# Performance work log

Measured on AMD Instinct MI355X. Metric: run time of the kernel, lower is better.

Reference implementation:

```python
import jax, jax.numpy as jnp
import numpy as np

N_NODES = 100000


def gcn_conv(x, W, b, src, tgt, n_nodes):
    """PyG GCNConv: add self-loops, symmetric deg^-1/2 normalization, then aggregate."""
    xw = x @ W  # [N, out]
    # degree including self-loop (edge weights are all 1)
    deg = jnp.zeros((n_nodes,), dtype=x.dtype).at[tgt].add(1.0) + 1.0
    dinv = deg ** -0.5
    norm = dinv[src] * dinv[tgt]  # [E]
    agg = jax.ops.segment_sum(xw[src] * norm[:, None], tgt, num_segments=n_nodes)
    # self-loop contribution: norm_ii = dinv_i^2
    return agg + xw * (dinv ** 2)[:, None] + b


def setup_inputs() -> dict:
    key = jax.random.key(0)
    ks = jax.random.split(key, 9)
    d_in, d_hid, d_out = 128, 128, 64
    x = jax.random.normal(ks[0], (N_NODES, d_in), dtype=jnp.float32)
    edge_index = jax.random.randint(ks[1], (2, 200000), 0, N_NODES)
    pos_edge_index = jax.random.randint(ks[2], (2, 500000), 0, N_NODES)
    s = lambda k, shape, fan: jax.random.normal(k, shape, dtype=jnp.float32) / np.sqrt(fan)
    return {
        "x": x,
        "edge_index": edge_index,
        "pos_edge_index": pos_edge_index,
        "W_init": s(ks[3], (d_in, d_in), d_in),
        "b_init": jnp.zeros((d_in,), dtype=jnp.float32),
        "W1": s(ks[4], (d_in, d_hid), d_in),
        "b1": jnp.zeros((d_hid,), dtype=jnp.float32),
        "W2": s(ks[5], (d_hid, d_out), d_hid),
        "b2": jnp.zeros((d_out,), dtype=jnp.float32),
    }


def reference(x, edge_index, pos_edge_index, W_init, b_init, W1, b1, W2, b2):
    n = x.shape[0]
    src, tgt = pos_edge_index[0], pos_edge_index[1]
    h = x @ W_init + b_init                      # init_linear
    h = gcn_conv(h, W1, b1, src, tgt, n)         # conv1
    h = jax.nn.relu(h)
    h = gcn_conv(h, W2, b2, src, tgt, n)         # conv2
    # edge dot-product scoring (use_bilinear=False)
    logits = jnp.sum(h[edge_index[0]] * h[edge_index[1]], axis=-1)  # [E_pred]
    return logits
```

## Files before the change

### kernel.cpp

```cpp
#include <hip/hip_runtime.h>


typedef __attribute__((ext_vector_type(8))) short short8;
typedef __attribute__((ext_vector_type(4))) float f32x4;

__device__ __forceinline__ ushort f2bf(float v) {
    unsigned u = __float_as_uint(v);
    return (ushort)((u + 0x7FFFu + ((u >> 16) & 1u)) >> 16);
}
__device__ __forceinline__ float bf2f(ushort b) {
    return __uint_as_float(((unsigned)b) << 16);
}
__device__ __forceinline__ float bflo(unsigned u) { return __uint_as_float(u << 16); }
__device__ __forceinline__ float bfhi(unsigned u) { return __uint_as_float(u & 0xFFFF0000u); }
__device__ __forceinline__ unsigned packbf(float x, float y) {
    return (unsigned)f2bf(x) | ((unsigned)f2bf(y) << 16);
}
__device__ __forceinline__ void split2(float v, ushort& h, ushort& l) {
    unsigned u = __float_as_uint(v);
    unsigned hb = (u + 0x7FFFu + ((u >> 16) & 1u)) & 0xFFFF0000u;
    h = (ushort)(hb >> 16);
    l = f2bf(v - __uint_as_float(hb));
}

__global__ void prep_kernel(const float* __restrict__ Wi, const float* __restrict__ W1,
                            const float* __restrict__ W2,
                            ushort* __restrict__ Ti, ushort* __restrict__ T1,
                            ushort* __restrict__ T2, int* __restrict__ zp, int ztot)
{
    int o = blockIdx.x * blockDim.x + threadIdx.x;
    if (o < ztot) zp[o] = 0;
    if (o < 16384) {
        int c = o >> 7, k = o & 127;
        Ti[o] = f2bf(Wi[(size_t)k * 128 + c]);
    } else if (o < 32768) {
        int p = o - 16384;
        int c = p >> 7, k = p & 127;
        T1[p] = f2bf(W1[(size_t)k * 128 + c]);
    } else if (o < 40960) {
        int p = o - 32768;
        int c = p >> 7, k = p & 127;
        T2[p] = f2bf(W2[(size_t)k * 64 + c]);
    }
}

__global__ void hist_kernel(const int* __restrict__ tgt, int* __restrict__ counts, int e) {
    int i = blockIdx.x * blockDim.x + threadIdx.x;
    if (i < e) atomicAdd(&counts[tgt[i]], 1);
}
__global__ __launch_bounds__(256)
void scan1_kernel(const int* __restrict__ counts, int* __restrict__ rowptr,
                  int* __restrict__ bsum, float* __restrict__ dinv, int n)
{
    __shared__ int sdata[256];
    const int t = threadIdx.x;
    const int base = blockIdx.x * 1024 + t * 4;
    int v[4];
#pragma unroll
    for (int i = 0; i < 4; i++) v[i] = (base + i < n) ? counts[base + i] : 0;
#pragma unroll
    for (int i = 0; i < 4; i++)
        if (base + i < n) dinv[base + i] = 1.0f / sqrtf((float)(v[i] + 1));
    int tsum = v[0] + v[1] + v[2] + v[3];
    sdata[t] = tsum;
    __syncthreads();
    for (int off = 1; off < 256; off <<= 1) {
        int x = (t >= off) ? sdata[t - off] : 0;
        __syncthreads();
        if (t >= off) sdata[t] += x;
        __syncthreads();
    }
    if (t == 255) bsum[blockIdx.x] = sdata[255];
    int run = sdata[t] - tsum;
#pragma unroll
    for (int i = 0; i < 4; i++) {
        if (base + i < n) rowptr[base + i] = run;
        run += v[i];
    }
}
__global__ __launch_bounds__(256)
void scan2_kernel(int* __restrict__ bsum, int nb)
{
    __shared__ int sdata[256];
    const int t = threadIdx.x;
    int v = (t < nb) ? bsum[t] : 0;
    sdata[t] = v;
    __syncthreads();
    for (int off = 1; off < 256; off <<= 1) {
        int x = (t >= off) ? sdata[t - off] : 0;
        __syncthreads();
        if (t >= off) sdata[t] += x;
        __syncthreads();
    }
    if (t < nb) bsum[t] = sdata[t] - v;
}
__global__ void scan3_kernel(int* __restrict__ rowptr, const int* __restrict__ bsum,
                             int n, int e_total)
{
    int i = blockIdx.x * blockDim.x + threadIdx.x;
    if (i < n) rowptr[i] += bsum[i >> 10];
    if (i == 0) rowptr[n] = e_total;
}
__global__ void scatter_kernel(const int* __restrict__ src, const int* __restrict__ tgt,
                               const float* __restrict__ dinv, const int* __restrict__ rowptr,
                               int* __restrict__ cursor, int2* __restrict__ ew, int e)
{
    int i = blockIdx.x * blockDim.x + threadIdx.x;
    if (i >= e) return;
    int s = src[i], t = tgt[i];
    int p = rowptr[t] + atomicAdd(&cursor[t], 1);
    ew[p] = make_int2(s, __float_as_int(dinv[s] * dinv[t]));
}

__global__ __launch_bounds__(256)
void fused_gemm01_kernel(const float* __restrict__ x,
                         const ushort* __restrict__ WTi, const ushort* __restrict__ WT1,
                         const float* __restrict__ bias, ushort* __restrict__ xw1, int M)
{
    __shared__ ushort raw[36864];
    ushort (*H0h)[128][8] = (ushort(*)[128][8])raw;
    ushort (*H0l)[128][8] = (ushort(*)[128][8])(raw + 16384);
    ushort (*Bs)[128][8]  = (ushort(*)[128][8])(raw + 32768);

    const int tid = threadIdx.x;
    const int row0 = blockIdx.x * 128;
    const int wv = tid >> 6;
    const int l  = tid & 63;
    const int lr = l & 15;
    const int lk = l >> 4;

    f32x4 acc0[8], acc1[8];
#pragma unroll
    for (int n = 0; n < 8; ++n) {
        acc0[n] = (f32x4){0.f, 0.f, 0.f, 0.f};
        acc1[n] = (f32x4){0.f, 0.f, 0.f, 0.f};
    }

    for (int kk = 0; kk < 128; kk += 32) {
        {
            const int r  = tid >> 1;
            const int kh = tid & 1;
            const int gr = row0 + r;
            float f[16];
            if (gr < M) {
                const float4* p = (const float4*)(x + (size_t)gr * 128 + kk + kh * 16);
                float4 q0 = p[0], q1 = p[1], q2 = p[2], q3 = p[3];
                f[0]=q0.x; f[1]=q0.y; f[2]=q0.z; f[3]=q0.w;
                f[4]=q1.x; f[5]=q1.y; f[6]=q1.z; f[7]=q1.w;
                f[8]=q2.x; f[9]=q2.y; f[10]=q2.z; f[11]=q2.w;
                f[12]=q3.x; f[13]=q3.y; f[14]=q3.z; f[15]=q3.w;
            } else {
#pragma unroll
                for (int j = 0; j < 16; j++) f[j] = 0.f;
            }
#pragma unroll
            for (int uu = 0; uu < 2; ++uu) {
                short8 hv, lv;
#pragma unroll
                for (int j = 0; j < 8; ++j) {
                    ushort h, lo;
                    split2(f[8 * uu + j], h, lo);
                    hv[j] = (short)h; lv[j] = (short)lo;
                }
                *(short8*)&H0h[2 * kh + uu][r][0] = hv;
                *(short8*)&H0l[2 * kh + uu][r][0] = lv;
            }
        }
        {
#pragma unroll
            for (int u = 0; u < 2; ++u) {
                const int unit = tid * 2 + u;
                const int c   = unit >> 2;
                const int kgl = unit & 3;
                *(short8*)&Bs[kgl][c][0] = *(const short8*)(WTi + (size_t)c * 128 + kk + 8 * kgl);
            }
        }
        __syncthreads();
        short8 ah0 = *(const short8*)&H0h[lk][wv * 32 + lr][0];
        short8 ah1 = *(const short8*)&H0h[lk][wv * 32 + 16 + lr][0];
        short8 al0 = *(const short8*)&H0l[lk][wv * 32 + lr][0];
        short8 al1 = *(const short8*)&H0l[lk][wv * 32 + 16 + lr][0];
#pragma unroll
        for (int n = 0; n < 8; ++n) {
            short8 bh = *(const short8*)&Bs[lk][n * 16 + lr][0];
            acc0[n] = __builtin_amdgcn_mfma_f32_16x16x32_bf16(bh, ah0, acc0[n], 0, 0, 0);
            acc1[n] = __builtin_amdgcn_mfma_f32_16x16x32_bf16(bh, ah1, acc1[n], 0, 0, 0);
            acc0[n] = __builtin_amdgcn_mfma_f32_16x16x32_bf16(bh, al0, acc0[n], 0, 0, 0);
            acc1[n] = __builtin_amdgcn_mfma_f32_16x16x32_bf16(bh, al1, acc1[n], 0, 0, 0);
        }
        __syncthreads();
    }

#pragma unroll
    for (int n = 0; n < 8; ++n) {
        const float4 b4 = *(const float4*)(bias + n * 16 + 4 * lk);
        const float bb[4] = {b4.x, b4.y, b4.z, b4.w};
        const int ks = 2 * n + (lk >> 1);
        const int jo = (lk & 1) * 4;
#pragma unroll
        for (int half = 0; half < 2; ++half) {
            const int m = wv * 32 + 16 * half + lr;
            uint2 uh, ul;
            unsigned hw[4], lw[4];
#pragma unroll
            for (int r = 0; r < 4; ++r) {
                ushort h, lo;
                split2((half ? acc1[n][r] : acc0[n][r]) + bb[r], h, lo);
                hw[r] = h; lw[r] = lo;
            }
            uh.x = hw[0] | (hw[1] << 16); uh.y = hw[2] | (hw[3] << 16);
            ul.x = lw[0] | (lw[1] << 16); ul.y = lw[2] | (lw[3] << 16);
            *(uint2*)&H0h[ks][m][jo] = uh;
            *(uint2*)&H0l[ks][m][jo] = ul;
        }
    }
    __syncthreads();

#pragma unroll
    for (int n = 0; n < 8; ++n) {
        acc0[n] = (f32x4){0.f, 0.f, 0.f, 0.f};
        acc1[n] = (f32x4){0.f, 0.f, 0.f, 0.f};
    }
    for (int kk = 0; kk < 4; ++kk) {
        {
#pragma unroll
            for (int u = 0; u < 2; ++u) {
                const int unit = tid * 2 + u;
                const int c   = unit >> 2;
                const int kgl = unit & 3;
                *(short8*)&Bs[kgl][c][0] = *(const short8*)(WT1 + (size_t)c * 128 + kk * 32 + 8 * kgl);
            }
        }
        __syncthreads();
        short8 ah0 = *(const short8*)&H0h[kk * 4 + lk][wv * 32 + lr][0];
        short8 ah1 = *(const short8*)&H0h[kk * 4 + lk][wv * 32 + 16 + lr][0];
        short8 al0 = *(const short8*)&H0l[kk * 4 + lk][wv * 32 + lr][0];
        short8 al1 = *(const short8*)&H0l[kk * 4 + lk][wv * 32 + 16 + lr][0];
#pragma unroll
        for (int n = 0; n < 8; ++n) {
            short8 bh = *(const short8*)&Bs[lk][n * 16 + lr][0];
            acc0[n] = __builtin_amdgcn_mfma_f32_16x16x32_bf16(bh, ah0, acc0[n], 0, 0, 0);
            acc1[n] = __builtin_amdgcn_mfma_f32_16x16x32_bf16(bh, ah1, acc1[n], 0, 0, 0);
            acc0[n] = __builtin_amdgcn_mfma_f32_16x16x32_bf16(bh, al0, acc0[n], 0, 0, 0);
            acc1[n] = __builtin_amdgcn_mfma_f32_16x16x32_bf16(bh, al1, acc1[n], 0, 0, 0);
        }
        __syncthreads();
    }

#pragma unroll
    for (int n = 0; n < 8; ++n) {
#pragma unroll
        for (int half = 0; half < 2; ++half) {
            const int m = row0 + wv * 32 + 16 * half + lr;
            if (m < M) {
                uint2 u;
                const f32x4 a = half ? acc1[n] : acc0[n];
                u.x = (unsigned)f2bf(a[0]) | ((unsigned)f2bf(a[1]) << 16);
                u.y = (unsigned)f2bf(a[2]) | ((unsigned)f2bf(a[3]) << 16);
                *(uint2*)(xw1 + (size_t)m * 128 + n * 16 + 4 * lk) = u;
            }
        }
    }
}

#define C1_CAP 1536

__device__ __forceinline__ void tile_add(unsigned* p, float ax, float ay) {
    unsigned old = *p;
    *p = packbf(bflo(old) + ax, bfhi(old) + ay);
}

__global__ __launch_bounds__(256)
void conv1_fused_kernel(const ushort* __restrict__ xw1, const float* __restrict__ dinv,
                        const int* __restrict__ rowptr, const int2* __restrict__ ew,
                        const float* __restrict__ b1, const ushort* __restrict__ WT2,
                        ushort* __restrict__ xw2, int N)
{
    __shared__ ushort tile[16][65][8];
    __shared__ int2 sew[C1_CAP];
    __shared__ int srp[65];

    const int tid  = threadIdx.x;
    const int n0   = blockIdx.x * 64;
    const int nc   = min(64, N - n0);
    const int wv   = tid >> 6;
    const int lane = tid & 63;

    if (tid <= nc) srp[tid] = rowptr[n0 + tid];
    __syncthreads();
    const int e0   = srp[0];
    const int etot = srp[nc] - e0;
    const int ecap = min(etot, C1_CAP);

    for (int i = tid; i < ecap; i += 256) {
        int2 d = ew[e0 + i];
        int idx = e0 + i;
        int lo = 0, hi = nc - 1;
        while (lo < hi) { int mid = (lo + hi + 1) >> 1; if (srp[mid] <= idx) lo = mid; else hi = mid - 1; }
        sew[i] = make_int2((d.x & 0xFFFFF) | (lo << 20), d.y);
    }

    const float bb0 = b1[2 * lane];
    const float bb1 = b1[2 * lane + 1];
    const int  kg = lane >> 2;
    const int  jj = (2 * lane) & 7;
    unsigned* tbase = (unsigned*)&tile[kg][0][jj];
    for (int r = wv; r < 64; r += 4) {
        float vx = 0.f, vy = 0.f;
        if (r < nc) {
            unsigned u = *(const unsigned*)(xw1 + (size_t)(n0 + r) * 128 + 2 * lane);
            float dt = dinv[n0 + r];
            float cc = dt * dt;
            vx = fmaf(bflo(u), cc, bb0);
            vy = fmaf(bfhi(u), cc, bb1);
        }
        tbase[r * 4] = packbf(vx, vy);
    }
    __syncthreads();

    const int nlo = wv * 16;
    if (nlo < nc) {
        const int nhi = min(nlo + 16, nc);
        int i = srp[nlo] - e0;
        const int iend_all = srp[nhi] - e0;
        const int iend = min(iend_all, ecap);
        float ax = 0.f, ay = 0.f;
        int cur = -1;

        for (; i + 8 <= iend; i += 8) {
            int2 d[8];
#pragma unroll
            for (int u = 0; u < 8; ++u) d[u] = sew[i + u];
            unsigned v[8];
#pragma unroll
            for (int u = 0; u < 8; ++u)
                v[u] = *(const unsigned*)(xw1 + (size_t)(((unsigned)d[u].x) & 0xFFFFFu) * 128 + 2 * lane);
#pragma unroll
            for (int u = 0; u < 8; ++u) {
                const int tg = (int)(((unsigned)d[u].x) >> 20);
                if (tg != cur) {
                    if (cur >= 0) tile_add(tbase + cur * 4, ax, ay);
                    cur = tg; ax = 0.f; ay = 0.f;
                }
                const float w = __int_as_float(d[u].y);
                ax = fmaf(bflo(v[u]), w, ax);
                ay = fmaf(bfhi(v[u]), w, ay);
            }
        }
        for (; i < iend; ++i) {
            int2 d = sew[i];
            unsigned v = *(const unsigned*)(xw1 + (size_t)(((unsigned)d.x) & 0xFFFFFu) * 128 + 2 * lane);
            const int tg = (int)(((unsigned)d.x) >> 20);
            if (tg != cur) {
                if (cur >= 0) tile_add(tbase + cur * 4, ax, ay);
                cur = tg; ax = 0.f; ay = 0.f;
            }
            const float w = __int_as_float(d.y);
            ax = fmaf(bflo(v), w, ax);
            ay = fmaf(bfhi(v), w, ay);
        }
        if (cur >= 0) tile_add(tbase + cur * 4, ax, ay);

        if (iend_all > ecap) {
            for (int nn = nlo; nn < nhi; ++nn) {
                int lo2 = max(srp[nn] - e0, ecap);
                int hi2 = srp[nn + 1] - e0;
                if (lo2 < hi2) {
                    ax = 0.f; ay = 0.f;
                    for (int t = lo2; t < hi2; ++t) {
                        int2 d = ew[e0 + t];
                        unsigned v = *(const unsigned*)(xw1 + (size_t)d.x * 128 + 2 * lane);
                        const float w = __int_as_float(d.y);
                        ax = fmaf(bflo(v), w, ax);
                        ay = fmaf(bfhi(v), w, ay);
                    }
                    tile_add(tbase + nn * 4, ax, ay);
                }
            }
        }
    }
    __syncthreads();

    const int lr = lane & 15;
    const int lk = lane >> 4;
    f32x4 acc[4];
#pragma unroll
    for (int n = 0; n < 4; ++n) acc[n] = (f32x4){0.f, 0.f, 0.f, 0.f};

    for (int kt = 0; kt < 4; ++kt) {
        short8 ah = *(const short8*)&tile[kt * 4 + lk][wv * 16 + lr][0];
#pragma unroll
        for (int j = 0; j < 8; ++j) {
            ushort vv = (ushort)ah[j];
            ah[j] = (short)((vv & 0x8000u) ? 0 : vv);
        }
#pragma unroll
        for (int n = 0; n < 4; ++n) {
            short8 bh = *(const short8*)(WT2 + (size_t)(n * 16 + lr) * 128 + kt * 32 + lk * 8);
            acc[n] = __builtin_amdgcn_mfma_f32_16x16x32_bf16(bh, ah, acc[n], 0, 0, 0);
        }
    }

    const int ml = wv * 16 + lr;
    if (ml < nc) {
        const size_t m = (size_t)(n0 + ml);
#pragma unroll
        for (int n = 0; n < 4; ++n) {
            uint2 u;
            u.x = (unsigned)f2bf(acc[n][0]) | ((unsigned)f2bf(acc[n][1]) << 16);
            u.y = (unsigned)f2bf(acc[n][2]) | ((unsigned)f2bf(acc[n][3]) << 16);
            *(uint2*)(xw2 + m * 64 + n * 16 + 4 * lk) = u;
        }
    }
}

__global__ __launch_bounds__(256)
void gather2_kernel(const ushort* __restrict__ xw, const float* __restrict__ dinv,
                    const int* __restrict__ rowptr, const int2* __restrict__ ew,
                    const float* __restrict__ bias, ushort* __restrict__ out, int n)
{
    const int node = blockIdx.x * 4 + (threadIdx.x >> 6);
    const int lane = threadIdx.x & 63;
    if (node >= n) return;
    const float dt = dinv[node];
    int j = rowptr[node];
    const int j1 = rowptr[node + 1];

    float acc = fmaf(bf2f(xw[(size_t)node * 64 + lane]), dt * dt, bias[lane]);
    for (; j + 3 < j1; j += 4) {
        const int2 p0 = ew[j], p1 = ew[j + 1], p2 = ew[j + 2], p3 = ew[j + 3];
        const float v0 = bf2f(xw[(size_t)p0.x * 64 + lane]);
        const float v1 = bf2f(xw[(size_t)p1.x * 64 + lane]);
        const float v2 = bf2f(xw[(size_t)p2.x * 64 + lane]);
        const float v3 = bf2f(xw[(size_t)p3.x * 64 + lane]);
        acc = fmaf(v0, __int_as_float(p0.y), acc);
        acc = fmaf(v1, __int_as_float(p1.y), acc);
        acc = fmaf(v2, __int_as_float(p2.y), acc);
        acc = fmaf(v3, __int_as_float(p3.y), acc);
    }
    for (; j < j1; ++j) {
        const int2 p0 = ew[j];
        acc = fmaf(bf2f(xw[(size_t)p0.x * 64 + lane]), __int_as_float(p0.y), acc);
    }
    out[(size_t)node * 64 + lane] = f2bf(acc);
}

__global__ void score_kernel(const ushort* __restrict__ h, const int* __restrict__ ea,
                             const int* __restrict__ eb, float* __restrict__ out, int E)
{
    long long gid = (long long)blockIdx.x * blockDim.x + threadIdx.x;
    int e = (int)(gid >> 3);
    int l = (int)(gid & 7);
    if (e >= E) return;
    int a = ea[e], b = eb[e];
    uint4 ua = *(const uint4*)(h + (size_t)a * 64 + 8 * l);
    uint4 ub = *(const uint4*)(h + (size_t)b * 64 + 8 * l);
    float s;
    s  = __uint_as_float(ua.x << 16)         * __uint_as_float(ub.x << 16);
    s += __uint_as_float(ua.x & 0xFFFF0000u) * __uint_as_float(ub.x & 0xFFFF0000u);
    s += __uint_as_float(ua.y << 16)         * __uint_as_float(ub.y << 16);
    s += __uint_as_float(ua.y & 0xFFFF0000u) * __uint_as_float(ub.y & 0xFFFF0000u);
    s += __uint_as_float(ua.z << 16)         * __uint_as_float(ub.z << 16);
    s += __uint_as_float(ua.z & 0xFFFF0000u) * __uint_as_float(ub.z & 0xFFFF0000u);
    s += __uint_as_float(ua.w << 16)         * __uint_as_float(ub.w << 16);
    s += __uint_as_float(ua.w & 0xFFFF0000u) * __uint_as_float(ub.w & 0xFFFF0000u);
    s += __shfl_xor(s, 4);
    s += __shfl_xor(s, 2);
    s += __shfl_xor(s, 1);
    if (l == 0) out[e] = s;
}

extern "C" void kernel_launch(void* const* d_in, const int* in_sizes, int n_in,
                              void* d_out, int out_size, void* d_ws, size_t ws_size,
                              hipStream_t stream)
{
    const float* x              = (const float*)d_in[0];
    const int*   edge_index     = (const int*)d_in[1];
    const int*   pos_edge_index = (const int*)d_in[2];
    const float* W_init         = (const float*)d_in[3];
    const float* b_init         = (const float*)d_in[4];
    const float* W1             = (const float*)d_in[5];
    const float* b1             = (const float*)d_in[6];
    const float* W2             = (const float*)d_in[7];
    const float* b2             = (const float*)d_in[8];
    float* out = (float*)d_out;

    const int N     = in_sizes[0] / 128;
    const int Epred = in_sizes[1] / 2;
    const int E     = in_sizes[2] / 2;

    const int* src = pos_edge_index;
    const int* tgt = pos_edge_index + E;
    const int* ea  = edge_index;
    const int* eb  = edge_index + Epred;

    int2*   ew   = (int2*)d_ws;
    ushort* regA = (ushort*)(ew + E);
    ushort* regB = regA + (size_t)N * 128;
    float*  dinv = (float*)(regB + (size_t)N * 128);
    int*   counts = (int*)(dinv + N);
    int*   cursor = counts + N;
    int*   rowptr = cursor + N;
    int*   bsum   = rowptr + N + 2;
    ushort* WTi = (ushort*)(((uintptr_t)(bsum + 256) + 15) & ~(uintptr_t)15);
    ushort* WT1 = WTi + 16384;
    ushort* WT2 = WT1 + 16384;

    ushort* xw1 = regA;
    ushort* xw2 = regB;
    ushort* h2  = regB + (size_t)N * 64;

    const int BLK = 256;
    const int nb  = (N + 1023) / 1024;

    prep_kernel<<<(2 * N + BLK - 1) / BLK, BLK, 0, stream>>>(
        W_init, W1, W2, WTi, WT1, WT2, counts, 2 * N);

    hist_kernel<<<(E + BLK - 1) / BLK, BLK, 0, stream>>>(tgt, counts, E);
    scan1_kernel<<<nb, 256, 0, stream>>>(counts, rowptr, bsum, dinv, N);
    scan2_kernel<<<1, 256, 0, stream>>>(bsum, nb);
    scan3_kernel<<<(N + BLK - 1) / BLK, BLK, 0, stream>>>(rowptr, bsum, N, E);
    scatter_kernel<<<(E + BLK - 1) / BLK, BLK, 0, stream>>>(src, tgt, dinv, rowptr, cursor, ew, E);

    fused_gemm01_kernel<<<(N + 127) / 128, BLK, 0, stream>>>(x, WTi, WT1, b_init, xw1, N);

    conv1_fused_kernel<<<(N + 63) / 64, BLK, 0, stream>>>(
        xw1, dinv, rowptr, ew, b1, WT2, xw2, N);

    gather2_kernel<<<(N + 3) / 4, BLK, 0, stream>>>(xw2, dinv, rowptr, ew, b2, h2, N);

    score_kernel<<<((long long)Epred * 8 + BLK - 1) / BLK, BLK, 0, stream>>>(
        h2, ea, eb, out, Epred);
}
```

Before: 192.6 us.

## Drop LDS edge staging in conv1 and widen gather2 unroll to eight

```diff
diff --git a/kernel.cpp b/kernel.cpp
--- a/kernel.cpp
+++ b/kernel.cpp
@@ -263,8 +263,6 @@
     }
 }
 
-#define C1_CAP 1536
-
 __device__ __forceinline__ void tile_add(unsigned* p, float ax, float ay) {
     unsigned old = *p;
     *p = packbf(bflo(old) + ax, bfhi(old) + ay);
@@ -277,7 +275,6 @@
                         ushort* __restrict__ xw2, int N)
 {
     __shared__ ushort tile[16][65][8];
-    __shared__ int2 sew[C1_CAP];
     __shared__ int srp[65];
 
     const int tid  = threadIdx.x;
@@ -287,18 +284,6 @@
     const int lane = tid & 63;
 
     if (tid <= nc) srp[tid] = rowptr[n0 + tid];
-    __syncthreads();
-    const int e0   = srp[0];
-    const int etot = srp[nc] - e0;
-    const int ecap = min(etot, C1_CAP);
-
-    for (int i = tid; i < ecap; i += 256) {
-        int2 d = ew[e0 + i];
-        int idx = e0 + i;
-        int lo = 0, hi = nc - 1;
-        while (lo < hi) { int mid = (lo + hi + 1) >> 1; if (srp[mid] <= idx) lo = mid; else hi = mid - 1; }
-        sew[i] = make_int2((d.x & 0xFFFFF) | (lo << 20), d.y);
-    }
 
     const float bb0 = b1[2 * lane];
     const float bb1 = b1[2 * lane + 1];
@@ -321,26 +306,29 @@
     const int nlo = wv * 16;
     if (nlo < nc) {
         const int nhi = min(nlo + 16, nc);
+        const int e0 = srp[0];
         int i = srp[nlo] - e0;
-        const int iend_all = srp[nhi] - e0;
-        const int iend = min(iend_all, ecap);
+        const int iend = srp[nhi] - e0;
+        int cur = nlo;
+        int nxt = srp[nlo + 1] - e0;
         float ax = 0.f, ay = 0.f;
-        int cur = -1;
 
         for (; i + 8 <= iend; i += 8) {
             int2 d[8];
 #pragma unroll
-            for (int u = 0; u < 8; ++u) d[u] = sew[i + u];
+            for (int u = 0; u < 8; ++u) d[u] = ew[e0 + i + u];
             unsigned v[8];
 #pragma unroll
             for (int u = 0; u < 8; ++u)
-                v[u] = *(const unsigned*)(xw1 + (size_t)(((unsigned)d[u].x) & 0xFFFFFu) * 128 + 2 * lane);
+                v[u] = *(const unsigned*)(xw1 + (size_t)d[u].x * 128 + 2 * lane);
 #pragma unroll
             for (int u = 0; u < 8; ++u) {
-                const int tg = (int)(((unsigned)d[u].x) >> 20);
-                if (tg != cur) {
-                    if (cur >= 0) tile_add(tbase + cur * 4, ax, ay);
-                    cur = tg; ax = 0.f; ay = 0.f;
+                const int idx = i + u;
+                while (idx >= nxt) {
+                    tile_add(tbase + cur * 4, ax, ay);
+                    ax = 0.f; ay = 0.f;
+                    ++cur;
+                    nxt = srp[cur + 1] - e0;
                 }
                 const float w = __int_as_float(d[u].y);
                 ax = fmaf(bflo(v[u]), w, ax);
@@ -348,36 +336,19 @@
             }
         }
         for (; i < iend; ++i) {
-            int2 d = sew[i];
-            unsigned v = *(const unsigned*)(xw1 + (size_t)(((unsigned)d.x) & 0xFFFFFu) * 128 + 2 * lane);
-            const int tg = (int)(((unsigned)d.x) >> 20);
-            if (tg != cur) {
-                if (cur >= 0) tile_add(tbase + cur * 4, ax, ay);
-                cur = tg; ax = 0.f; ay = 0.f;
+            int2 d = ew[e0 + i];
+            unsigned v = *(const unsigned*)(xw1 + (size_t)d.x * 128 + 2 * lane);
+            while (i >= nxt) {
+                tile_add(tbase + cur * 4, ax, ay);
+                ax = 0.f; ay = 0.f;
+                ++cur;
+                nxt = srp[cur + 1] - e0;
             }
             const float w = __int_as_float(d.y);
             ax = fmaf(bflo(v), w, ax);
             ay = fmaf(bfhi(v), w, ay);
         }
-        if (cur >= 0) tile_add(tbase + cur * 4, ax, ay);
-
-        if (iend_all > ecap) {
-            for (int nn = nlo; nn < nhi; ++nn) {
-                int lo2 = max(srp[nn] - e0, ecap);
-                int hi2 = srp[nn + 1] - e0;
-                if (lo2 < hi2) {
-                    ax = 0.f; ay = 0.f;
-                    for (int t = lo2; t < hi2; ++t) {
-                        int2 d = ew[e0 + t];
-                        unsigned v = *(const unsigned*)(xw1 + (size_t)d.x * 128 + 2 * lane);
-                        const float w = __int_as_float(d.y);
-                        ax = fmaf(bflo(v), w, ax);
-                        ay = fmaf(bfhi(v), w, ay);
-                    }
-                    tile_add(tbase + nn * 4, ax, ay);
-                }
-            }
-        }
+        tile_add(tbase + cur * 4, ax, ay);
     }
     __syncthreads();
 
@@ -427,16 +398,15 @@
     const int j1 = rowptr[node + 1];
 
     float acc = fmaf(bf2f(xw[(size_t)node * 64 + lane]), dt * dt, bias[lane]);
-    for (; j + 3 < j1; j += 4) {
-        const int2 p0 = ew[j], p1 = ew[j + 1], p2 = ew[j + 2], p3 = ew[j + 3];
-        const float v0 = bf2f(xw[(size_t)p0.x * 64 + lane]);
-        const float v1 = bf2f(xw[(size_t)p1.x * 64 + lane]);
-        const float v2 = bf2f(xw[(size_t)p2.x * 64 + lane]);
-        const float v3 = bf2f(xw[(size_t)p3.x * 64 + lane]);
-        acc = fmaf(v0, __int_as_float(p0.y), acc);
-        acc = fmaf(v1, __int_as_float(p1.y), acc);
-        acc = fmaf(v2, __int_as_float(p2.y), acc);
-        acc = fmaf(v3, __int_as_float(p3.y), acc);
+    for (; j + 8 <= j1; j += 8) {
+        int2 d[8];
+#pragma unroll
+        for (int u = 0; u < 8; ++u) d[u] = ew[j + u];
+        float v[8];
+#pragma unroll
+        for (int u = 0; u < 8; ++u) v[u] = bf2f(xw[(size_t)d[u].x * 64 + lane]);
+#pragma unroll
+        for (int u = 0; u < 8; ++u) acc = fmaf(v[u], __int_as_float(d[u].y), acc);
     }
     for (; j < j1; ++j) {
         const int2 p0 = ew[j];
```

New measurement: 197.2 us. +2.4%, slower.
